# Kernel optimization log

Hardware: AMD Instinct MI355X
Metric: run time of the kernel (lower is better)

## Reference

```python
import jax, jax.numpy as jnp
import numpy as np


def setup_inputs() -> dict:
    key = jax.random.key(0)
    N = 100000
    x = jax.random.normal(key, (N,), dtype=jnp.float32)
    return {"x": x, "f_true": 90, "fs": 100000, "delta": 3, "f_min": 40, "f_max": 240}


def reference(x, f_true, fs, delta, f_min, f_max):
    # PSD(f) = (sum_i x[i] cos(2*pi*f*i/fs))^2 + (sum_i x[i] sin(2*pi*f*i/fs))^2
    # evaluated at integer frequencies f in [f_min, f_max]; loss = -10*log10(sum_wanted / sum_unwanted)
    N = x.shape[0]
    freqs = jnp.arange(f_min, f_max + 1)                      # [F] int bins
    t = jnp.arange(N, dtype=jnp.float32)                      # [N]
    ang = (2.0 * jnp.pi / fs) * freqs.astype(jnp.float32)[:, None] * t[None, :]  # [F, N]
    real = jnp.cos(ang) @ x                                   # [F]
    imag = jnp.sin(ang) @ x                                   # [F]
    psd = real * real + imag * imag                           # [F]
    wanted = (freqs >= f_true - delta) & (freqs <= f_true + delta)
    term1 = jnp.sum(jnp.where(wanted, psd, 0.0))
    term2 = jnp.sum(jnp.where(wanted, 0.0, psd))
    return -10.0 * jnp.log10(term1 / term2)
```

## Files before the change

### kernel.cpp

```cpp
#include <hip/hip_runtime.h>
#include <math.h>

#define BLK   256
#define MAXF  512
#define SPLIT 4

__device__ __forceinline__ unsigned umod_fast(unsigned a, unsigned fs, float inv_fs) {
    unsigned q = (unsigned)((float)a * inv_fs);
    int r = (int)a - (int)(q * fs);
    if (r < 0) r += (int)fs;
    if (r < 0) r += (int)fs;
    if (r >= (int)fs) r -= (int)fs;
    if (r >= (int)fs) r -= (int)fs;
    return (unsigned)r;
}

__global__ void __launch_bounds__(BLK) dft_proj_kernel(
    const float* __restrict__ x, int N,
    const int* __restrict__ p_fs,
    const int* __restrict__ p_fmin,
    const int* __restrict__ p_fmax,
    float* __restrict__ ws)
{
    const unsigned fs   = (unsigned)*p_fs;
    const int      fmin = *p_fmin;
    const int      fmax = *p_fmax;
    const int      F    = fmax - fmin + 1;
    const float  inv_fs = 1.0f / (float)fs;

    int Nc = (N + SPLIT - 1) / SPLIT;
    Nc = (Nc + 3) & ~3;
    const int W = F * SPLIT;

    float* re = ws;
    float* im = ws + MAXF * SPLIT;

    __shared__ float red[8];

    for (int w = blockIdx.x; w < W; w += gridDim.x) {
        const int j     = w >> 2;
        const int chunk = w & (SPLIT - 1);
        if (j >= MAXF) break;

        const unsigned f   = (unsigned)(fmin + j);
        const int      tid = threadIdx.x;
        const int      cs   = chunk * Nc;
        const int      iend = min(N, cs + Nc);

        const unsigned kb = (unsigned)(((unsigned long long)f * (unsigned)cs) % fs);
        unsigned pt = umod_fast(f * (unsigned)(4 * tid), fs, inv_fs);
        unsigned k0 = kb + pt; if (k0 >= fs) k0 -= fs;
        const unsigned k4 = (unsigned)(((unsigned long long)f * (unsigned)(4 * BLK)) % fs);
        const unsigned kf = (f >= fs) ? (f % fs) : f;

        float cA = __builtin_amdgcn_cosf((float)k0 * inv_fs);
        float sA = __builtin_amdgcn_sinf((float)k0 * inv_fs);
        const float C4 = __builtin_amdgcn_cosf((float)k4 * inv_fs);
        const float S4 = __builtin_amdgcn_sinf((float)k4 * inv_fs);
        float cB = fmaf(cA, C4, -(sA * S4));
        float sB = fmaf(sA, C4,  (cA * S4));
        const float C8 = fmaf(C4, C4, -(S4 * S4));
        const float S8 = 2.0f * C4 * S4;

        float a0r = 0.f, a0i = 0.f, a1r = 0.f, a1i = 0.f;
        float a2r = 0.f, a2i = 0.f, a3r = 0.f, a3i = 0.f;

        int b = cs + 4 * tid;
        for (; b + 4 * BLK + 4 <= iend; b += 8 * BLK) {
            float4 xa = *reinterpret_cast<const float4*>(x + b);
            float4 xb = *reinterpret_cast<const float4*>(x + b + 4 * BLK);
            a0r = fmaf(xa.x, cA, a0r); a0i = fmaf(xa.x, sA, a0i);
            a1r = fmaf(xa.y, cA, a1r); a1i = fmaf(xa.y, sA, a1i);
            a2r = fmaf(xa.z, cA, a2r); a2i = fmaf(xa.z, sA, a2i);
            a3r = fmaf(xa.w, cA, a3r); a3i = fmaf(xa.w, sA, a3i);
            a0r = fmaf(xb.x, cB, a0r); a0i = fmaf(xb.x, sB, a0i);
            a1r = fmaf(xb.y, cB, a1r); a1i = fmaf(xb.y, sB, a1i);
            a2r = fmaf(xb.z, cB, a2r); a2i = fmaf(xb.z, sB, a2i);
            a3r = fmaf(xb.w, cB, a3r); a3i = fmaf(xb.w, sB, a3i);
            float cn = fmaf(cA, C8, -(sA * S8));
            float sn = fmaf(sA, C8,  (cA * S8));
            cA = cn; sA = sn;
            cn = fmaf(cB, C8, -(sB * S8));
            sn = fmaf(sB, C8,  (cB * S8));
            cB = cn; sB = sn;
        }
        #pragma unroll
        for (int p = 0; p < 4; ++p) {
            int idx = b + p;
            if (idx < iend) {
                float xv = x[idx];
                if (p == 0) { a0r = fmaf(xv, cA, a0r); a0i = fmaf(xv, sA, a0i); }
                if (p == 1) { a1r = fmaf(xv, cA, a1r); a1i = fmaf(xv, sA, a1i); }
                if (p == 2) { a2r = fmaf(xv, cA, a2r); a2i = fmaf(xv, sA, a2i); }
                if (p == 3) { a3r = fmaf(xv, cA, a3r); a3i = fmaf(xv, sA, a3i); }
            }
        }
        #pragma unroll
        for (int p = 0; p < 4; ++p) {
            int idx = b + 4 * BLK + p;
            if (idx < iend) {
                float xv = x[idx];
                if (p == 0) { a0r = fmaf(xv, cB, a0r); a0i = fmaf(xv, sB, a0i); }
                if (p == 1) { a1r = fmaf(xv, cB, a1r); a1i = fmaf(xv, sB, a1i); }
                if (p == 2) { a2r = fmaf(xv, cB, a2r); a2i = fmaf(xv, sB, a2i); }
                if (p == 3) { a3r = fmaf(xv, cB, a3r); a3i = fmaf(xv, sB, a3i); }
            }
        }

        const float c1 = __builtin_amdgcn_cosf((float)kf * inv_fs);
        const float s1 = __builtin_amdgcn_sinf((float)kf * inv_fs);
        const float c2 = fmaf(c1, c1, -(s1 * s1));
        const float s2 = 2.0f * c1 * s1;
        const float c3 = fmaf(c2, c1, -(s2 * s1));
        const float s3 = fmaf(s2, c1,  (c2 * s1));
        float arS = a0r, aiS = a0i;
        arS = fmaf(c1, a1r, arS); arS = fmaf(-s1, a1i, arS);
        aiS = fmaf(c1, a1i, aiS); aiS = fmaf( s1, a1r, aiS);
        arS = fmaf(c2, a2r, arS); arS = fmaf(-s2, a2i, arS);
        aiS = fmaf(c2, a2i, aiS); aiS = fmaf( s2, a2r, aiS);
        arS = fmaf(c3, a3r, arS); arS = fmaf(-s3, a3i, arS);
        aiS = fmaf(c3, a3i, aiS); aiS = fmaf( s3, a3r, aiS);

        #pragma unroll
        for (int o = 32; o > 0; o >>= 1) {
            arS += __shfl_down(arS, o, 64);
            aiS += __shfl_down(aiS, o, 64);
        }
        const int lane = tid & 63;
        const int wid  = tid >> 6;
        if (lane == 0) { red[wid * 2] = arS; red[wid * 2 + 1] = aiS; }
        __syncthreads();
        if (tid == 0) {
            re[w] = (red[0] + red[2]) + (red[4] + red[6]);
            im[w] = (red[1] + red[3]) + (red[5] + red[7]);
        }
        __syncthreads();
    }
}

__global__ void __launch_bounds__(BLK) loss_kernel(
    const float* __restrict__ ws,
    const int* __restrict__ p_ftrue,
    const int* __restrict__ p_delta,
    const int* __restrict__ p_fmin,
    const int* __restrict__ p_fmax,
    float* __restrict__ out)
{
    const int ftrue = *p_ftrue;
    const int delta = *p_delta;
    const int fmin  = *p_fmin;
    const int fmax  = *p_fmax;
    const int F     = fmax - fmin + 1;

    float t1 = 0.0f, t2 = 0.0f;
    for (int j = threadIdx.x; j < F && j < MAXF; j += BLK) {
        float r = 0.0f, m = 0.0f;
        #pragma unroll
        for (int u = 0; u < SPLIT; ++u) {
            r += ws[j * SPLIT + u];
            m += ws[MAXF * SPLIT + j * SPLIT + u];
        }
        float psd = r * r + m * m;
        int   fq  = fmin + j;
        bool wanted = (fq >= ftrue - delta) && (fq <= ftrue + delta);
        if (wanted) t1 += psd; else t2 += psd;
    }

    __shared__ float red[8];
    #pragma unroll
    for (int o = 32; o > 0; o >>= 1) {
        t1 += __shfl_down(t1, o, 64);
        t2 += __shfl_down(t2, o, 64);
    }
    const int lane = threadIdx.x & 63;
    const int wid  = threadIdx.x >> 6;
    if (lane == 0) { red[wid * 2] = t1; red[wid * 2 + 1] = t2; }
    __syncthreads();
    if (threadIdx.x == 0) {
        float a = (red[0] + red[2]) + (red[4] + red[6]);
        float b = (red[1] + red[3]) + (red[5] + red[7]);
        out[0] = -10.0f * log10f(a / b);
    }
}

extern "C" void kernel_launch(void* const* d_in, const int* in_sizes, int n_in,
                              void* d_out, int out_size, void* d_ws, size_t ws_size,
                              hipStream_t stream) {
    const float* x       = (const float*)d_in[0];
    const int*   p_ftrue = (const int*)d_in[1];
    const int*   p_fs    = (const int*)d_in[2];
    const int*   p_delta = (const int*)d_in[3];
    const int*   p_fmin  = (const int*)d_in[4];
    const int*   p_fmax  = (const int*)d_in[5];
    float*       out     = (float*)d_out;
    float*       ws      = (float*)d_ws;
    const int N = in_sizes[0];

    dft_proj_kernel<<<1024, BLK, 0, stream>>>(x, N, p_fs, p_fmin, p_fmax, ws);
    loss_kernel<<<1, BLK, 0, stream>>>(ws, p_ftrue, p_delta, p_fmin, p_fmax, out);
}
```

Before: 12.58 us.

## Fuse DFT projection and loss into one kernel with last-block atomic reduction

Merges the two kernels into one. Each 1024-thread block computes one frequency bin over the whole signal, with no chunk split, and writes its PSD through an atomic. The last block to finish, detected by an atomic counter, computes the final loss. This removes the second kernel launch and the partial-sum workspace, but adds a memset launch and runs 201 large blocks instead of 804 smaller work items, which may reduce parallelism.

```diff
diff --git a/kernel.cpp b/kernel.cpp
--- a/kernel.cpp
+++ b/kernel.cpp
@@ -1,9 +1,9 @@
 #include <hip/hip_runtime.h>
 #include <math.h>
 
-#define BLK   256
+#define BLK   1024
 #define MAXF  512
-#define SPLIT 4
+#define NW    (BLK / 64)
 
 __device__ __forceinline__ unsigned umod_fast(unsigned a, unsigned fs, float inv_fs) {
     unsigned q = (unsigned)((float)a * inv_fs);
@@ -15,43 +15,40 @@
     return (unsigned)r;
 }
 
-__global__ void __launch_bounds__(BLK) dft_proj_kernel(
+__global__ void __launch_bounds__(BLK) extractor_kernel(
     const float* __restrict__ x, int N,
+    const int* __restrict__ p_ftrue,
     const int* __restrict__ p_fs,
+    const int* __restrict__ p_delta,
     const int* __restrict__ p_fmin,
     const int* __restrict__ p_fmax,
-    float* __restrict__ ws)
+    unsigned* __restrict__ wsu,
+    float* __restrict__ out)
 {
     const unsigned fs   = (unsigned)*p_fs;
     const int      fmin = *p_fmin;
     const int      fmax = *p_fmax;
-    const int      F    = fmax - fmin + 1;
-    const float  inv_fs = 1.0f / (float)fs;
+    int F = fmax - fmin + 1;
+    if (F > MAXF) F = MAXF;
+    const float inv_fs = 1.0f / (float)fs;
 
-    int Nc = (N + SPLIT - 1) / SPLIT;
-    Nc = (Nc + 3) & ~3;
-    const int W = F * SPLIT;
+    unsigned* counter = wsu;
+    unsigned* psd_u   = wsu + 64;
 
-    float* re = ws;
-    float* im = ws + MAXF * SPLIT;
+    __shared__ float    red[2 * NW];
+    __shared__ unsigned s_last;
 
-    __shared__ float red[8];
+    const int tid  = threadIdx.x;
+    const int lane = tid & 63;
+    const int wid  = tid >> 6;
 
-    for (int w = blockIdx.x; w < W; w += gridDim.x) {
-        const int j     = w >> 2;
-        const int chunk = w & (SPLIT - 1);
-        if (j >= MAXF) break;
+    for (int j = blockIdx.x; j < F; j += gridDim.x) {
+        const unsigned f = (unsigned)(fmin + j);
 
-        const unsigned f   = (unsigned)(fmin + j);
-        const int      tid = threadIdx.x;
-        const int      cs   = chunk * Nc;
-        const int      iend = min(N, cs + Nc);
-
-        const unsigned kb = (unsigned)(((unsigned long long)f * (unsigned)cs) % fs);
-        unsigned pt = umod_fast(f * (unsigned)(4 * tid), fs, inv_fs);
-        unsigned k0 = kb + pt; if (k0 >= fs) k0 -= fs;
-        const unsigned k4 = (unsigned)(((unsigned long long)f * (unsigned)(4 * BLK)) % fs);
-        const unsigned kf = (f >= fs) ? (f % fs) : f;
+        const unsigned k0 = umod_fast(f * (unsigned)(4 * tid), fs, inv_fs);
+        const unsigned k4 = umod_fast(f * (unsigned)(4 * BLK), fs, inv_fs);
+        unsigned k8 = k4 + k4; if (k8 >= fs) k8 -= fs;
+        const unsigned kf = umod_fast(f, fs, inv_fs);
 
         float cA = __builtin_amdgcn_cosf((float)k0 * inv_fs);
         float sA = __builtin_amdgcn_sinf((float)k0 * inv_fs);
@@ -59,14 +56,14 @@
         const float S4 = __builtin_amdgcn_sinf((float)k4 * inv_fs);
         float cB = fmaf(cA, C4, -(sA * S4));
         float sB = fmaf(sA, C4,  (cA * S4));
-        const float C8 = fmaf(C4, C4, -(S4 * S4));
-        const float S8 = 2.0f * C4 * S4;
+        const float C8 = __builtin_amdgcn_cosf((float)k8 * inv_fs);
+        const float S8 = __builtin_amdgcn_sinf((float)k8 * inv_fs);
 
         float a0r = 0.f, a0i = 0.f, a1r = 0.f, a1i = 0.f;
         float a2r = 0.f, a2i = 0.f, a3r = 0.f, a3i = 0.f;
 
-        int b = cs + 4 * tid;
-        for (; b + 4 * BLK + 4 <= iend; b += 8 * BLK) {
+        int b = 4 * tid;
+        for (; b + 4 * BLK + 4 <= N; b += 8 * BLK) {
             float4 xa = *reinterpret_cast<const float4*>(x + b);
             float4 xb = *reinterpret_cast<const float4*>(x + b + 4 * BLK);
             a0r = fmaf(xa.x, cA, a0r); a0i = fmaf(xa.x, sA, a0i);
@@ -87,7 +84,7 @@
         #pragma unroll
         for (int p = 0; p < 4; ++p) {
             int idx = b + p;
-            if (idx < iend) {
+            if (idx < N) {
                 float xv = x[idx];
                 if (p == 0) { a0r = fmaf(xv, cA, a0r); a0i = fmaf(xv, sA, a0i); }
                 if (p == 1) { a1r = fmaf(xv, cA, a1r); a1i = fmaf(xv, sA, a1i); }
@@ -98,7 +95,7 @@
         #pragma unroll
         for (int p = 0; p < 4; ++p) {
             int idx = b + 4 * BLK + p;
-            if (idx < iend) {
+            if (idx < N) {
                 float xv = x[idx];
                 if (p == 0) { a0r = fmaf(xv, cB, a0r); a0i = fmaf(xv, sB, a0i); }
                 if (p == 1) { a1r = fmaf(xv, cB, a1r); a1i = fmaf(xv, sB, a1i); }
@@ -126,60 +123,46 @@
             arS += __shfl_down(arS, o, 64);
             aiS += __shfl_down(aiS, o, 64);
         }
-        const int lane = tid & 63;
-        const int wid  = tid >> 6;
         if (lane == 0) { red[wid * 2] = arS; red[wid * 2 + 1] = aiS; }
         __syncthreads();
         if (tid == 0) {
-            re[w] = (red[0] + red[2]) + (red[4] + red[6]);
-            im[w] = (red[1] + red[3]) + (red[5] + red[7]);
+            float r = 0.f, m = 0.f;
+            #pragma unroll
+            for (int u = 0; u < NW; ++u) { r += red[u * 2]; m += red[u * 2 + 1]; }
+            float psd = r * r + m * m;
+            unsigned oldx = atomicExch(&psd_u[j], __float_as_uint(psd));
+            asm volatile("" :: "v"(oldx));
+            asm volatile("s_waitcnt vmcnt(0)" ::: "memory");
+            unsigned oldc = atomicAdd(counter, 1u);
+            s_last = (oldc + 1u == (unsigned)F) ? 1u : 0u;
         }
         __syncthreads();
-    }
-}
 
-__global__ void __launch_bounds__(BLK) loss_kernel(
-    const float* __restrict__ ws,
-    const int* __restrict__ p_ftrue,
-    const int* __restrict__ p_delta,
-    const int* __restrict__ p_fmin,
-    const int* __restrict__ p_fmax,
-    float* __restrict__ out)
-{
-    const int ftrue = *p_ftrue;
-    const int delta = *p_delta;
-    const int fmin  = *p_fmin;
-    const int fmax  = *p_fmax;
-    const int F     = fmax - fmin + 1;
-
-    float t1 = 0.0f, t2 = 0.0f;
-    for (int j = threadIdx.x; j < F && j < MAXF; j += BLK) {
-        float r = 0.0f, m = 0.0f;
-        #pragma unroll
-        for (int u = 0; u < SPLIT; ++u) {
-            r += ws[j * SPLIT + u];
-            m += ws[MAXF * SPLIT + j * SPLIT + u];
+        if (s_last) {
+            const int ftrue = *p_ftrue;
+            const int delta = *p_delta;
+            float t1 = 0.f, t2 = 0.f;
+            for (int q = tid; q < F; q += BLK) {
+                float psd = __uint_as_float(atomicOr(&psd_u[q], 0u));
+                int   fq  = fmin + q;
+                bool wanted = (fq >= ftrue - delta) && (fq <= ftrue + delta);
+                if (wanted) t1 += psd; else t2 += psd;
+            }
+            #pragma unroll
+            for (int o = 32; o > 0; o >>= 1) {
+                t1 += __shfl_down(t1, o, 64);
+                t2 += __shfl_down(t2, o, 64);
+            }
+            if (lane == 0) { red[wid * 2] = t1; red[wid * 2 + 1] = t2; }
+            __syncthreads();
+            if (tid == 0) {
+                float a = 0.f, bb = 0.f;
+                #pragma unroll
+                for (int u = 0; u < NW; ++u) { a += red[u * 2]; bb += red[u * 2 + 1]; }
+                out[0] = -10.0f * log10f(a / bb);
+            }
         }
-        float psd = r * r + m * m;
-        int   fq  = fmin + j;
-        bool wanted = (fq >= ftrue - delta) && (fq <= ftrue + delta);
-        if (wanted) t1 += psd; else t2 += psd;
-    }
-
-    __shared__ float red[8];
-    #pragma unroll
-    for (int o = 32; o > 0; o >>= 1) {
-        t1 += __shfl_down(t1, o, 64);
-        t2 += __shfl_down(t2, o, 64);
-    }
-    const int lane = threadIdx.x & 63;
-    const int wid  = threadIdx.x >> 6;
-    if (lane == 0) { red[wid * 2] = t1; red[wid * 2 + 1] = t2; }
-    __syncthreads();
-    if (threadIdx.x == 0) {
-        float a = (red[0] + red[2]) + (red[4] + red[6]);
-        float b = (red[1] + red[3]) + (red[5] + red[7]);
-        out[0] = -10.0f * log10f(a / b);
+        __syncthreads();
     }
 }
 
@@ -193,9 +176,10 @@
     const int*   p_fmin  = (const int*)d_in[4];
     const int*   p_fmax  = (const int*)d_in[5];
     float*       out     = (float*)d_out;
-    float*       ws      = (float*)d_ws;
+    unsigned*    wsu     = (unsigned*)d_ws;
     const int N = in_sizes[0];
 
-    dft_proj_kernel<<<1024, BLK, 0, stream>>>(x, N, p_fs, p_fmin, p_fmax, ws);
-    loss_kernel<<<1, BLK, 0, stream>>>(ws, p_ftrue, p_delta, p_fmin, p_fmax, out);
+    hipMemsetAsync(d_ws, 0, sizeof(unsigned), stream);
+    extractor_kernel<<<256, BLK, 0, stream>>>(
+        x, N, p_ftrue, p_fs, p_delta, p_fmin, p_fmax, wsu, out);
 }
```

New measurement: 18.91 us. 1.5x slower.

## Process four frequencies per block to reuse loaded samples across bins

Applied to the files above, without the earlier changes.

Each block now handles a group of four frequency bins over one chunk of the signal, so every float4 of x loaded feeds four sets of accumulators instead of one. The signal split goes from 4 to 16 chunks, which keeps the number of work items high (ngrp*16 ≈ 816). Per-bin rotation constants now come from direct sin/cos of the reduced index rather than angle doubling. The cost is more registers per thread and a MAXF cap lowered to 256, which silently truncates larger frequency ranges.

```diff
diff --git a/kernel.cpp b/kernel.cpp
--- a/kernel.cpp
+++ b/kernel.cpp
@@ -2,8 +2,9 @@
 #include <math.h>
 
 #define BLK   256
-#define MAXF  512
-#define SPLIT 4
+#define MAXF  256
+#define SPLIT 16
+#define FPB   4
 
 __device__ __forceinline__ unsigned umod_fast(unsigned a, unsigned fs, float inv_fs) {
     unsigned q = (unsigned)((float)a * inv_fs);
@@ -25,74 +26,94 @@
     const unsigned fs   = (unsigned)*p_fs;
     const int      fmin = *p_fmin;
     const int      fmax = *p_fmax;
-    const int      F    = fmax - fmin + 1;
-    const float  inv_fs = 1.0f / (float)fs;
+    int F = fmax - fmin + 1;
+    if (F > MAXF) F = MAXF;
+    const float inv_fs = 1.0f / (float)fs;
 
     int Nc = (N + SPLIT - 1) / SPLIT;
     Nc = (Nc + 3) & ~3;
-    const int W = F * SPLIT;
+    const int ngrp = (F + FPB - 1) / FPB;
+    const int W    = ngrp * SPLIT;
 
     float* re = ws;
     float* im = ws + MAXF * SPLIT;
 
-    __shared__ float red[8];
+    __shared__ float red[FPB * 8];
+
+    const int tid  = threadIdx.x;
+    const int lane = tid & 63;
+    const int wid  = tid >> 6;
 
     for (int w = blockIdx.x; w < W; w += gridDim.x) {
-        const int j     = w >> 2;
+        const int gi    = w >> 4;
         const int chunk = w & (SPLIT - 1);
-        if (j >= MAXF) break;
-
-        const unsigned f   = (unsigned)(fmin + j);
-        const int      tid = threadIdx.x;
-        const int      cs   = chunk * Nc;
-        const int      iend = min(N, cs + Nc);
-
-        const unsigned kb = (unsigned)(((unsigned long long)f * (unsigned)cs) % fs);
-        unsigned pt = umod_fast(f * (unsigned)(4 * tid), fs, inv_fs);
-        unsigned k0 = kb + pt; if (k0 >= fs) k0 -= fs;
-        const unsigned k4 = (unsigned)(((unsigned long long)f * (unsigned)(4 * BLK)) % fs);
-        const unsigned kf = (f >= fs) ? (f % fs) : f;
-
-        float cA = __builtin_amdgcn_cosf((float)k0 * inv_fs);
-        float sA = __builtin_amdgcn_sinf((float)k0 * inv_fs);
-        const float C4 = __builtin_amdgcn_cosf((float)k4 * inv_fs);
-        const float S4 = __builtin_amdgcn_sinf((float)k4 * inv_fs);
-        float cB = fmaf(cA, C4, -(sA * S4));
-        float sB = fmaf(sA, C4,  (cA * S4));
-        const float C8 = fmaf(C4, C4, -(S4 * S4));
-        const float S8 = 2.0f * C4 * S4;
-
-        float a0r = 0.f, a0i = 0.f, a1r = 0.f, a1i = 0.f;
-        float a2r = 0.f, a2i = 0.f, a3r = 0.f, a3i = 0.f;
+        const int j0    = gi * FPB;
+        const int cs    = chunk * Nc;
+        const int iend  = min(N, cs + Nc);
+
+        float cA[FPB], sA[FPB], cB[FPB], sB[FPB], C8[FPB], S8[FPB];
+        float c1[FPB], s1[FPB];
+        float a0r[FPB], a0i[FPB], a1r[FPB], a1i[FPB];
+        float a2r[FPB], a2i[FPB], a3r[FPB], a3i[FPB];
+
+        #pragma unroll
+        for (int g = 0; g < FPB; ++g) {
+            int jg = j0 + g; if (jg >= F) jg = F - 1;
+            const unsigned f = (unsigned)(fmin + jg);
+            const unsigned kb = (unsigned)(((unsigned long long)f * (unsigned)cs) % fs);
+            unsigned pt = umod_fast(f * (unsigned)(4 * tid), fs, inv_fs);
+            unsigned k0 = kb + pt; if (k0 >= fs) k0 -= fs;
+            const unsigned k4 = umod_fast(f * (unsigned)(4 * BLK), fs, inv_fs);
+            unsigned k8 = k4 + k4; if (k8 >= fs) k8 -= fs;
+            const unsigned kf = umod_fast(f, fs, inv_fs);
+            cA[g] = __builtin_amdgcn_cosf((float)k0 * inv_fs);
+            sA[g] = __builtin_amdgcn_sinf((float)k0 * inv_fs);
+            const float C4 = __builtin_amdgcn_cosf((float)k4 * inv_fs);
+            const float S4 = __builtin_amdgcn_sinf((float)k4 * inv_fs);
+            cB[g] = fmaf(cA[g], C4, -(sA[g] * S4));
+            sB[g] = fmaf(sA[g], C4,  (cA[g] * S4));
+            C8[g] = __builtin_amdgcn_cosf((float)k8 * inv_fs);
+            S8[g] = __builtin_amdgcn_sinf((float)k8 * inv_fs);
+            c1[g] = __builtin_amdgcn_cosf((float)kf * inv_fs);
+            s1[g] = __builtin_amdgcn_sinf((float)kf * inv_fs);
+            a0r[g] = 0.f; a0i[g] = 0.f; a1r[g] = 0.f; a1i[g] = 0.f;
+            a2r[g] = 0.f; a2i[g] = 0.f; a3r[g] = 0.f; a3i[g] = 0.f;
+        }
 
         int b = cs + 4 * tid;
         for (; b + 4 * BLK + 4 <= iend; b += 8 * BLK) {
             float4 xa = *reinterpret_cast<const float4*>(x + b);
             float4 xb = *reinterpret_cast<const float4*>(x + b + 4 * BLK);
-            a0r = fmaf(xa.x, cA, a0r); a0i = fmaf(xa.x, sA, a0i);
-            a1r = fmaf(xa.y, cA, a1r); a1i = fmaf(xa.y, sA, a1i);
-            a2r = fmaf(xa.z, cA, a2r); a2i = fmaf(xa.z, sA, a2i);
-            a3r = fmaf(xa.w, cA, a3r); a3i = fmaf(xa.w, sA, a3i);
-            a0r = fmaf(xb.x, cB, a0r); a0i = fmaf(xb.x, sB, a0i);
-            a1r = fmaf(xb.y, cB, a1r); a1i = fmaf(xb.y, sB, a1i);
-            a2r = fmaf(xb.z, cB, a2r); a2i = fmaf(xb.z, sB, a2i);
-            a3r = fmaf(xb.w, cB, a3r); a3i = fmaf(xb.w, sB, a3i);
-            float cn = fmaf(cA, C8, -(sA * S8));
-            float sn = fmaf(sA, C8,  (cA * S8));
-            cA = cn; sA = sn;
-            cn = fmaf(cB, C8, -(sB * S8));
-            sn = fmaf(sB, C8,  (cB * S8));
-            cB = cn; sB = sn;
+            #pragma unroll
+            for (int g = 0; g < FPB; ++g) {
+                a0r[g] = fmaf(xa.x, cA[g], a0r[g]); a0i[g] = fmaf(xa.x, sA[g], a0i[g]);
+                a1r[g] = fmaf(xa.y, cA[g], a1r[g]); a1i[g] = fmaf(xa.y, sA[g], a1i[g]);
+                a2r[g] = fmaf(xa.z, cA[g], a2r[g]); a2i[g] = fmaf(xa.z, sA[g], a2i[g]);
+                a3r[g] = fmaf(xa.w, cA[g], a3r[g]); a3i[g] = fmaf(xa.w, sA[g], a3i[g]);
+                a0r[g] = fmaf(xb.x, cB[g], a0r[g]); a0i[g] = fmaf(xb.x, sB[g], a0i[g]);
+                a1r[g] = fmaf(xb.y, cB[g], a1r[g]); a1i[g] = fmaf(xb.y, sB[g], a1i[g]);
+                a2r[g] = fmaf(xb.z, cB[g], a2r[g]); a2i[g] = fmaf(xb.z, sB[g], a2i[g]);
+                a3r[g] = fmaf(xb.w, cB[g], a3r[g]); a3i[g] = fmaf(xb.w, sB[g], a3i[g]);
+                float cn = fmaf(cA[g], C8[g], -(sA[g] * S8[g]));
+                float sn = fmaf(sA[g], C8[g],  (cA[g] * S8[g]));
+                cA[g] = cn; sA[g] = sn;
+                cn = fmaf(cB[g], C8[g], -(sB[g] * S8[g]));
+                sn = fmaf(sB[g], C8[g],  (cB[g] * S8[g]));
+                cB[g] = cn; sB[g] = sn;
+            }
         }
         #pragma unroll
         for (int p = 0; p < 4; ++p) {
             int idx = b + p;
             if (idx < iend) {
                 float xv = x[idx];
-                if (p == 0) { a0r = fmaf(xv, cA, a0r); a0i = fmaf(xv, sA, a0i); }
-                if (p == 1) { a1r = fmaf(xv, cA, a1r); a1i = fmaf(xv, sA, a1i); }
-                if (p == 2) { a2r = fmaf(xv, cA, a2r); a2i = fmaf(xv, sA, a2i); }
-                if (p == 3) { a3r = fmaf(xv, cA, a3r); a3i = fmaf(xv, sA, a3i); }
+                #pragma unroll
+                for (int g = 0; g < FPB; ++g) {
+                    if (p == 0) { a0r[g] = fmaf(xv, cA[g], a0r[g]); a0i[g] = fmaf(xv, sA[g], a0i[g]); }
+                    if (p == 1) { a1r[g] = fmaf(xv, cA[g], a1r[g]); a1i[g] = fmaf(xv, sA[g], a1i[g]); }
+                    if (p == 2) { a2r[g] = fmaf(xv, cA[g], a2r[g]); a2i[g] = fmaf(xv, sA[g], a2i[g]); }
+                    if (p == 3) { a3r[g] = fmaf(xv, cA[g], a3r[g]); a3i[g] = fmaf(xv, sA[g], a3i[g]); }
+                }
             }
         }
         #pragma unroll
@@ -100,39 +121,49 @@
             int idx = b + 4 * BLK + p;
             if (idx < iend) {
                 float xv = x[idx];
-                if (p == 0) { a0r = fmaf(xv, cB, a0r); a0i = fmaf(xv, sB, a0i); }
-                if (p == 1) { a1r = fmaf(xv, cB, a1r); a1i = fmaf(xv, sB, a1i); }
-                if (p == 2) { a2r = fmaf(xv, cB, a2r); a2i = fmaf(xv, sB, a2i); }
-                if (p == 3) { a3r = fmaf(xv, cB, a3r); a3i = fmaf(xv, sB, a3i); }
-            }
-        }
-
-        const float c1 = __builtin_amdgcn_cosf((float)kf * inv_fs);
-        const float s1 = __builtin_amdgcn_sinf((float)kf * inv_fs);
-        const float c2 = fmaf(c1, c1, -(s1 * s1));
-        const float s2 = 2.0f * c1 * s1;
-        const float c3 = fmaf(c2, c1, -(s2 * s1));
-        const float s3 = fmaf(s2, c1,  (c2 * s1));
-        float arS = a0r, aiS = a0i;
-        arS = fmaf(c1, a1r, arS); arS = fmaf(-s1, a1i, arS);
-        aiS = fmaf(c1, a1i, aiS); aiS = fmaf( s1, a1r, aiS);
-        arS = fmaf(c2, a2r, arS); arS = fmaf(-s2, a2i, arS);
-        aiS = fmaf(c2, a2i, aiS); aiS = fmaf( s2, a2r, aiS);
-        arS = fmaf(c3, a3r, arS); arS = fmaf(-s3, a3i, arS);
-        aiS = fmaf(c3, a3i, aiS); aiS = fmaf( s3, a3r, aiS);
-
-        #pragma unroll
-        for (int o = 32; o > 0; o >>= 1) {
-            arS += __shfl_down(arS, o, 64);
-            aiS += __shfl_down(aiS, o, 64);
-        }
-        const int lane = tid & 63;
-        const int wid  = tid >> 6;
-        if (lane == 0) { red[wid * 2] = arS; red[wid * 2 + 1] = aiS; }
+                #pragma unroll
+                for (int g = 0; g < FPB; ++g) {
+                    if (p == 0) { a0r[g] = fmaf(xv, cB[g], a0r[g]); a0i[g] = fmaf(xv, sB[g], a0i[g]); }
+                    if (p == 1) { a1r[g] = fmaf(xv, cB[g], a1r[g]); a1i[g] = fmaf(xv, sB[g], a1i[g]); }
+                    if (p == 2) { a2r[g] = fmaf(xv, cB[g], a2r[g]); a2i[g] = fmaf(xv, sB[g], a2i[g]); }
+                    if (p == 3) { a3r[g] = fmaf(xv, cB[g], a3r[g]); a3i[g] = fmaf(xv, sB[g], a3i[g]); }
+                }
+            }
+        }
+
+        #pragma unroll
+        for (int g = 0; g < FPB; ++g) {
+            const float c2 = fmaf(c1[g], c1[g], -(s1[g] * s1[g]));
+            const float s2 = 2.0f * c1[g] * s1[g];
+            const float c3 = fmaf(c2, c1[g], -(s2 * s1[g]));
+            const float s3 = fmaf(s2, c1[g],  (c2 * s1[g]));
+            float arS = a0r[g], aiS = a0i[g];
+            arS = fmaf(c1[g], a1r[g], arS); arS = fmaf(-s1[g], a1i[g], arS);
+            aiS = fmaf(c1[g], a1i[g], aiS); aiS = fmaf( s1[g], a1r[g], aiS);
+            arS = fmaf(c2, a2r[g], arS); arS = fmaf(-s2, a2i[g], arS);
+            aiS = fmaf(c2, a2i[g], aiS); aiS = fmaf( s2, a2r[g], aiS);
+            arS = fmaf(c3, a3r[g], arS); arS = fmaf(-s3, a3i[g], arS);
+            aiS = fmaf(c3, a3i[g], aiS); aiS = fmaf( s3, a3r[g], aiS);
+            #pragma unroll
+            for (int o = 32; o > 0; o >>= 1) {
+                arS += __shfl_down(arS, o, 64);
+                aiS += __shfl_down(aiS, o, 64);
+            }
+            if (lane == 0) { red[g * 8 + wid * 2] = arS; red[g * 8 + wid * 2 + 1] = aiS; }
+        }
         __syncthreads();
-        if (tid == 0) {
-            re[w] = (red[0] + red[2]) + (red[4] + red[6]);
-            im[w] = (red[1] + red[3]) + (red[5] + red[7]);
+        if (tid < FPB) {
+            const int jg = j0 + tid;
+            if (jg < F) {
+                float r = 0.f, m = 0.f;
+                #pragma unroll
+                for (int u = 0; u < 4; ++u) {
+                    r += red[tid * 8 + u * 2];
+                    m += red[tid * 8 + u * 2 + 1];
+                }
+                re[jg * SPLIT + chunk] = r;
+                im[jg * SPLIT + chunk] = m;
+            }
         }
         __syncthreads();
     }
@@ -150,10 +181,11 @@
     const int delta = *p_delta;
     const int fmin  = *p_fmin;
     const int fmax  = *p_fmax;
-    const int F     = fmax - fmin + 1;
+    int F = fmax - fmin + 1;
+    if (F > MAXF) F = MAXF;
 
     float t1 = 0.0f, t2 = 0.0f;
-    for (int j = threadIdx.x; j < F && j < MAXF; j += BLK) {
+    for (int j = threadIdx.x; j < F; j += BLK) {
         float r = 0.0f, m = 0.0f;
         #pragma unroll
         for (int u = 0; u < SPLIT; ++u) {
```

Result: slower. 14.63 us (+16.4%).
